# Performance work log

Measured on AMD Instinct MI355X. Metric: run time of the kernel, lower is better.

Reference implementation:

```python
import jax, jax.numpy as jnp
import numpy as np

N_NODES = 50000


def _sage_layer(h, src, dst, W_self, W_neigh, b):
    # DGL SAGEConv with 'mean' aggregator: fc_self(h) + fc_neigh(mean_{u in N(v)} h_u) + b
    msg = h[src]                                             # [E, d] gather
    agg = jax.ops.segment_sum(msg, dst, num_segments=N_NODES)  # [N, d]
    deg = jax.ops.segment_sum(jnp.ones((src.shape[0], 1), h.dtype), dst, num_segments=N_NODES)
    mean = agg / jnp.maximum(deg, 1.0)
    return h @ W_self + mean @ W_neigh + b


def _edge_mlp(h, src, dst, Wp1, bp1, Wp2, bp2):
    # MLPPredictor: score(u,v) = W2 relu(W1 [h_u ; h_v])
    z = jnp.concatenate([h[src], h[dst]], axis=-1)           # [Ep, 2*out]
    hdn = jax.nn.relu(z @ Wp1 + bp1)
    return (hdn @ Wp2 + bp2)[:, 0]                           # [Ep]


def setup_inputs() -> dict:
    key = jax.random.key(0)
    ks = jax.random.split(key, 16)
    N, E, EP = N_NODES, 160000, 100000
    d_in, d_h, d_out = 512, 256, 64

    def glorot(k, shape):
        fan = shape[0] + shape[1]
        return jax.random.normal(k, shape, jnp.float32) * jnp.sqrt(2.0 / fan)

    return {
        "x": jax.random.normal(ks[0], (N, d_in), jnp.float32),
        "edge_src": jax.random.randint(ks[1], (E,), 0, N, jnp.int32),
        "edge_dst": jax.random.randint(ks[2], (E,), 0, N, jnp.int32),
        "pos_src": jax.random.randint(ks[3], (EP,), 0, N, jnp.int32),
        "pos_dst": jax.random.randint(ks[4], (EP,), 0, N, jnp.int32),
        "neg_src": jax.random.randint(ks[5], (EP,), 0, N, jnp.int32),
        "neg_dst": jax.random.randint(ks[6], (EP,), 0, N, jnp.int32),
        "W_self1": glorot(ks[7], (d_in, d_h)),
        "W_neigh1": glorot(ks[8], (d_in, d_h)),
        "b1": jnp.zeros((d_h,), jnp.float32),
        "W_self2": glorot(ks[9], (d_h, d_out)),
        "W_neigh2": glorot(ks[10], (d_h, d_out)),
        "b2": jnp.zeros((d_out,), jnp.float32),
        "Wp1": glorot(ks[11], (2 * d_out, d_out)),
        "bp1": jnp.zeros((d_out,), jnp.float32),
        "Wp2": glorot(ks[12], (d_out, 1)),
        "bp2": jnp.zeros((1,), jnp.float32),
    }


def reference(x, edge_src, edge_dst, pos_src, pos_dst, neg_src, neg_dst,
              W_self1, W_neigh1, b1, W_self2, W_neigh2, b2, Wp1, bp1, Wp2, bp2):
    # 2-layer SAGE (512 -> 256 -> 64), relu between layers
    h = jax.nn.relu(_sage_layer(x, edge_src, edge_dst, W_self1, W_neigh1, b1))
    h = _sage_layer(h, edge_src, edge_dst, W_self2, W_neigh2, b2)
    pos_score = _edge_mlp(h, pos_src, pos_dst, Wp1, bp1, Wp2, bp2)
    neg_score = _edge_mlp(h, neg_src, neg_dst, Wp1, bp1, Wp2, bp2)
    return (pos_score, neg_score)
```

## Files before the change

### kernel.cpp

```cpp
#include <hip/hip_runtime.h>

#define NN 50000
#define NE 160000
#define NP 100000
#define DIN 512
#define DH  256
#define DO  64
#define NBLK_SCAN 196

#define PW1_BLKS 1024
#define PW2_BLKS 128
#define PWP_BLKS 32
#define ZDEG_BLKS 196
#define PREP_BLKS (PW1_BLKS + PW2_BLKS + PWP_BLKS + ZDEG_BLKS)

typedef short bf16x8 __attribute__((ext_vector_type(8)));
typedef float f32x4  __attribute__((ext_vector_type(4)));

__device__ __forceinline__ float bf2f(unsigned short u) {
    return __uint_as_float(((unsigned int)u) << 16);
}
__device__ __forceinline__ unsigned short f2bf(float f) {
    unsigned int x = __float_as_uint(f);
    return (unsigned short)((x + 0x7fffu + ((x >> 16) & 1u)) >> 16);
}

__device__ __forceinline__ void gload_lds16(const void* g, void* l) {
    __builtin_amdgcn_global_load_lds(
        (const __attribute__((address_space(1))) void*)g,
        (__attribute__((address_space(3))) void*)l, 16, 0, 0);
}

__global__ __launch_bounds__(256) void prep_all(
    const float* __restrict__ Wself1, const float* __restrict__ Wneigh1, unsigned short* __restrict__ Bt1,
    const float* __restrict__ Wself2, const float* __restrict__ Wneigh2, unsigned short* __restrict__ Bt2,
    const float* __restrict__ Wp1, unsigned short* __restrict__ Wp1b,
    int* __restrict__ deg_i)
{
    int blk = blockIdx.x;
    if (blk < PW1_BLKS) {
        int idx = blk * 256 + threadIdx.x;
        int n = idx >> 9, k = idx & 511;
        float v = (n < DH) ? Wself1[(size_t)k * DH + n] : Wneigh1[(size_t)k * DH + (n - DH)];
        Bt1[idx] = f2bf(v);
        return;
    }
    blk -= PW1_BLKS;
    if (blk < PW2_BLKS) {
        int idx = blk * 256 + threadIdx.x;
        int n = idx >> 8, k = idx & 255;
        float v = (n < DO) ? Wself2[(size_t)k * DO + n] : Wneigh2[(size_t)k * DO + (n - DO)];
        Bt2[idx] = f2bf(v);
        return;
    }
    blk -= PW2_BLKS;
    if (blk < PWP_BLKS) {
        int idx = blk * 256 + threadIdx.x;
        int n = idx >> 7, k = idx & 127;
        Wp1b[idx] = f2bf(Wp1[(size_t)k * 64 + n]);
        return;
    }
    blk -= PWP_BLKS;
    {
        int i = blk * 256 + threadIdx.x;
        if (i < 50048) deg_i[i] = 0;
    }
}

__global__ __launch_bounds__(256) void deg_count(const int* __restrict__ dst, int* __restrict__ deg) {
    int e = blockIdx.x * 256 + threadIdx.x;
    if (e < NE) atomicAdd(&deg[dst[e]], 1);
}

__global__ __launch_bounds__(256) void scan_part(const int* __restrict__ deg, int* __restrict__ excl,
                                                 int* __restrict__ bsums) {
    __shared__ int sh[256];
    int i = blockIdx.x * 256 + threadIdx.x;
    int v = (i < NN) ? deg[i] : 0;
    sh[threadIdx.x] = v;
    __syncthreads();
    #pragma unroll
    for (int off = 1; off < 256; off <<= 1) {
        int t = (threadIdx.x >= off) ? sh[threadIdx.x - off] : 0;
        __syncthreads();
        sh[threadIdx.x] += t;
        __syncthreads();
    }
    if (i < NN) excl[i] = sh[threadIdx.x] - v;
    if (threadIdx.x == 255) bsums[blockIdx.x] = sh[255];
}

__global__ __launch_bounds__(256) void scan_sums(int* __restrict__ bsums, int* __restrict__ boff) {
    __shared__ int sh[256];
    int v = (threadIdx.x < NBLK_SCAN) ? bsums[threadIdx.x] : 0;
    sh[threadIdx.x] = v;
    __syncthreads();
    #pragma unroll
    for (int off = 1; off < 256; off <<= 1) {
        int t = (threadIdx.x >= off) ? sh[threadIdx.x - off] : 0;
        __syncthreads();
        sh[threadIdx.x] += t;
        __syncthreads();
    }
    boff[threadIdx.x] = sh[threadIdx.x] - v;
}

__global__ __launch_bounds__(256) void scan_add(int* __restrict__ off, const int* __restrict__ boff,
                                                int* __restrict__ cursor) {
    int i = blockIdx.x * 256 + threadIdx.x;
    if (i < NN) {
        int o = off[i] + boff[blockIdx.x];
        off[i] = o;
        cursor[i] = o;
    }
    if (i == 0) off[NN] = NE;
}

__global__ __launch_bounds__(256) void fill_csr(const int* __restrict__ src, const int* __restrict__ dst,
                                                int* __restrict__ cursor, int* __restrict__ eidx) {
    int e = blockIdx.x * 256 + threadIdx.x;
    if (e < NE) {
        int p = atomicAdd(&cursor[dst[e]], 1);
        eidx[p] = src[e];
    }
}

__global__ __launch_bounds__(256) void gemm_xf32(
    const float* __restrict__ A, const unsigned short* __restrict__ Bt,
    unsigned short* __restrict__ Cout, int M, int N, int K)
{
    __shared__ unsigned short As[2][128 * 64];
    __shared__ unsigned short Bs[2][128 * 64];
    const int tid = threadIdx.x;
    const int w = tid >> 6, l = tid & 63;
    const int wr = (w >> 1) * 64, wc = (w & 1) * 64;

    const int nwg = gridDim.x, gx = N >> 7;
    const int q = nwg >> 3, r = nwg & 7;
    const int xcd = blockIdx.x & 7, pos = blockIdx.x >> 3;
    const int work = (xcd < r ? xcd * (q + 1) : r * (q + 1) + (xcd - r) * q) + pos;
    const int row0 = (work / gx) * 128, col0 = (work % gx) * 128;

    f32x4 acc[4][4];
    #pragma unroll
    for (int i = 0; i < 4; ++i)
        #pragma unroll
        for (int j = 0; j < 4; ++j)
            #pragma unroll
            for (int rr = 0; rr < 4; ++rr) acc[i][j][rr] = 0.0f;

    const int wave_lds_chunk = (tid & 192) * 8;

    float4 pa[4][2];

#define LOAD_PA(K0)                                                          \
    {                                                                        \
        _Pragma("unroll")                                                    \
        for (int u = 0; u < 4; ++u) {                                        \
            int c = u * 256 + tid;                                           \
            int row_ = c >> 3, j_ = c & 7;                                   \
            int grow = row0 + row_; if (grow >= M) grow = M - 1;             \
            const float* s = A + (size_t)grow * K + (K0) + j_ * 8;           \
            pa[u][0] = *(const float4*)s;                                    \
            pa[u][1] = *(const float4*)(s + 4);                              \
        }                                                                    \
    }

#define WRITE_A(BUF)                                                         \
    {                                                                        \
        _Pragma("unroll")                                                    \
        for (int u = 0; u < 4; ++u) {                                        \
            int c = u * 256 + tid;                                           \
            int row_ = c >> 3, j_ = c & 7;                                   \
            int js_ = j_ ^ (row_ & 7);                                       \
            union { bf16x8 v; unsigned int u32[4]; } pk;                     \
            asm("v_cvt_pk_bf16_f32 %0, %1, %2" : "=v"(pk.u32[0]) : "v"(pa[u][0].x), "v"(pa[u][0].y)); \
            asm("v_cvt_pk_bf16_f32 %0, %1, %2" : "=v"(pk.u32[1]) : "v"(pa[u][0].z), "v"(pa[u][0].w)); \
            asm("v_cvt_pk_bf16_f32 %0, %1, %2" : "=v"(pk.u32[2]) : "v"(pa[u][1].x), "v"(pa[u][1].y)); \
            asm("v_cvt_pk_bf16_f32 %0, %1, %2" : "=v"(pk.u32[3]) : "v"(pa[u][1].z), "v"(pa[u][1].w)); \
            *(bf16x8*)&As[BUF][row_ * 64 + js_ * 8] = pk.v;                  \
        }                                                                    \
    }

#define STAGE_B(BUF, K0)                                                     \
    {                                                                        \
        _Pragma("unroll")                                                    \
        for (int u = 0; u < 4; ++u) {                                        \
            int c = u * 256 + tid;                                           \
            int cn = c >> 3, j_ = c & 7;                                     \
            int js_ = j_ ^ (cn & 7);                                         \
            gload_lds16(Bt + (size_t)(col0 + cn) * K + (K0) + js_ * 8,       \
                        (void*)(Bs[BUF] + (u * 256) * 8 + wave_lds_chunk));  \
        }                                                                    \
    }

    LOAD_PA(0);
    STAGE_B(0, 0);
    WRITE_A(0);
    LOAD_PA(64);
    __syncthreads();

    int cur = 0;
    for (int k0 = 0; k0 < K; k0 += 64) {
        const int nxt = k0 + 64;
        if (nxt < K) {
            STAGE_B(cur ^ 1, nxt);
            WRITE_A(cur ^ 1);
            if (nxt + 64 < K) LOAD_PA(nxt + 64);
        }

        #pragma unroll
        for (int kk = 0; kk < 2; ++kk) {
            bf16x8 af[4], bfv[4];
            #pragma unroll
            for (int i = 0; i < 4; ++i) {
                int row = wr + i * 16 + (l & 15);
                int ch = (kk * 4 + (l >> 4)) ^ (row & 7);
                af[i] = *(const bf16x8*)&As[cur][row * 64 + ch * 8];
            }
            #pragma unroll
            for (int j = 0; j < 4; ++j) {
                int cc = wc + j * 16 + (l & 15);
                int ch = (kk * 4 + (l >> 4)) ^ (cc & 7);
                bfv[j] = *(const bf16x8*)&Bs[cur][cc * 64 + ch * 8];
            }
            #pragma unroll
            for (int i = 0; i < 4; ++i)
                #pragma unroll
                for (int j = 0; j < 4; ++j)
                    acc[i][j] = __builtin_amdgcn_mfma_f32_16x16x32_bf16(af[i], bfv[j], acc[i][j], 0, 0, 0);
        }
        __syncthreads();
        cur ^= 1;
    }
#undef LOAD_PA
#undef WRITE_A
#undef STAGE_B

    #pragma unroll
    for (int i = 0; i < 4; ++i) {
        #pragma unroll
        for (int j = 0; j < 4; ++j) {
            int r0 = row0 + wr + i * 16 + ((l >> 4) << 2);
            int c  = col0 + wc + j * 16 + (l & 15);
            #pragma unroll
            for (int rr = 0; rr < 4; ++rr) {
                if (r0 + rr < M)
                    Cout[(size_t)(r0 + rr) * N + c] = f2bf(acc[i][j][rr]);
            }
        }
    }
}

__global__ __launch_bounds__(256) void gemm_bf16(
    const unsigned short* __restrict__ A, const unsigned short* __restrict__ Bt,
    unsigned short* __restrict__ Cout, int M, int N, int K)
{
    __shared__ unsigned short As[128 * 64];
    __shared__ unsigned short Bs[128 * 64];
    const int tid = threadIdx.x;
    const int w = tid >> 6, l = tid & 63;
    const int wr = (w >> 1) * 64, wc = (w & 1) * 64;

    const int nwg = gridDim.x, gx = N >> 7;
    const int q = nwg >> 3, r = nwg & 7;
    const int xcd = blockIdx.x & 7, pos = blockIdx.x >> 3;
    const int work = (xcd < r ? xcd * (q + 1) : r * (q + 1) + (xcd - r) * q) + pos;
    const int row0 = (work / gx) * 128, col0 = (work % gx) * 128;

    f32x4 acc[4][4];
    #pragma unroll
    for (int i = 0; i < 4; ++i)
        #pragma unroll
        for (int j = 0; j < 4; ++j)
            #pragma unroll
            for (int rr = 0; rr < 4; ++rr) acc[i][j][rr] = 0.0f;

    const int wave_lds_chunk = (tid & 192) * 8;

    for (int k0 = 0; k0 < K; k0 += 64) {
        __syncthreads();
        #pragma unroll
        for (int u = 0; u < 4; ++u) {
            int c = u * 256 + tid;
            int row = c >> 3, j = c & 7;
            int js = j ^ (row & 7);
            int grow = row0 + row; if (grow >= M) grow = M - 1;
            gload_lds16(A + (size_t)grow * K + k0 + js * 8,
                        (void*)(As + (u * 256) * 8 + wave_lds_chunk));
        }
        #pragma unroll
        for (int u = 0; u < 4; ++u) {
            int c = u * 256 + tid;
            int cn = c >> 3, j = c & 7;
            int js = j ^ (cn & 7);
            gload_lds16(Bt + (size_t)(col0 + cn) * K + k0 + js * 8,
                        (void*)(Bs + (u * 256) * 8 + wave_lds_chunk));
        }
        __syncthreads();

        #pragma unroll
        for (int kk = 0; kk < 2; ++kk) {
            bf16x8 af[4], bfv[4];
            #pragma unroll
            for (int i = 0; i < 4; ++i) {
                int row = wr + i * 16 + (l & 15);
                int ch = (kk * 4 + (l >> 4)) ^ (row & 7);
                af[i] = *(const bf16x8*)&As[row * 64 + ch * 8];
            }
            #pragma unroll
            for (int j = 0; j < 4; ++j) {
                int cc = wc + j * 16 + (l & 15);
                int ch = (kk * 4 + (l >> 4)) ^ (cc & 7);
                bfv[j] = *(const bf16x8*)&Bs[cc * 64 + ch * 8];
            }
            #pragma unroll
            for (int i = 0; i < 4; ++i)
                #pragma unroll
                for (int j = 0; j < 4; ++j)
                    acc[i][j] = __builtin_amdgcn_mfma_f32_16x16x32_bf16(af[i], bfv[j], acc[i][j], 0, 0, 0);
        }
    }

    #pragma unroll
    for (int i = 0; i < 4; ++i) {
        #pragma unroll
        for (int j = 0; j < 4; ++j) {
            int r0 = row0 + wr + i * 16 + ((l >> 4) << 2);
            int c  = col0 + wc + j * 16 + (l & 15);
            #pragma unroll
            for (int rr = 0; rr < 4; ++rr) {
                if (r0 + rr < M)
                    Cout[(size_t)(r0 + rr) * N + c] = f2bf(acc[i][j][rr]);
            }
        }
    }
}

__global__ __launch_bounds__(256) void agg_combine256(
    const unsigned short* __restrict__ C1, const int* __restrict__ off, const int* __restrict__ eidx,
    const float* __restrict__ b, unsigned short* __restrict__ h1b)
{
    const int wave = threadIdx.x >> 6, lane = threadIdx.x & 63;
    const int n = blockIdx.x * 4 + wave;
    if (n >= NN) return;
    const int e0 = off[n], e1 = off[n + 1];
    float acc0 = 0.f, acc1 = 0.f, acc2 = 0.f, acc3 = 0.f;
    for (int e = e0; e < e1; ++e) {
        int s = eidx[e];
        ushort4 v = *(const ushort4*)&C1[(size_t)s * 512 + 256 + lane * 4];
        acc0 += bf2f(v.x); acc1 += bf2f(v.y); acc2 += bf2f(v.z); acc3 += bf2f(v.w);
    }
    const float rd = (e1 > e0) ? 1.0f / (float)(e1 - e0) : 1.0f;
    ushort4 sv = *(const ushort4*)&C1[(size_t)n * 512 + lane * 4];
    float4 bb = ((const float4*)b)[lane];
    ushort4 o;
    o.x = f2bf(fmaxf(bf2f(sv.x) + acc0 * rd + bb.x, 0.f));
    o.y = f2bf(fmaxf(bf2f(sv.y) + acc1 * rd + bb.y, 0.f));
    o.z = f2bf(fmaxf(bf2f(sv.z) + acc2 * rd + bb.z, 0.f));
    o.w = f2bf(fmaxf(bf2f(sv.w) + acc3 * rd + bb.w, 0.f));
    *(ushort4*)&h1b[(size_t)n * 256 + lane * 4] = o;
}

__global__ __launch_bounds__(256) void agg_combine64(
    const unsigned short* __restrict__ C2, const int* __restrict__ off, const int* __restrict__ eidx,
    const float* __restrict__ b, unsigned short* __restrict__ h2b)
{
    const int wave = threadIdx.x >> 6, lane = threadIdx.x & 63;
    const int n = blockIdx.x * 4 + wave;
    if (n >= NN) return;
    const int e0 = off[n], e1 = off[n + 1];
    float acc = 0.f;
    for (int e = e0; e < e1; ++e) {
        int s = eidx[e];
        acc += bf2f(C2[(size_t)s * 128 + 64 + lane]);
    }
    const float rd = (e1 > e0) ? 1.0f / (float)(e1 - e0) : 1.0f;
    h2b[(size_t)n * 64 + lane] = f2bf(bf2f(C2[(size_t)n * 128 + lane]) + acc * rd + b[lane]);
}

__global__ __launch_bounds__(256) void edge_mlp_mfma(
    const unsigned short* __restrict__ h2b,
    const int* __restrict__ psrc, const int* __restrict__ pdst,
    const int* __restrict__ nsrc, const int* __restrict__ ndst,
    const unsigned short* __restrict__ Wp1b, const float* __restrict__ bp1,
    const float* __restrict__ Wp2, const float* __restrict__ bp2,
    float* __restrict__ out)
{
    __shared__ unsigned short z[128 * 128];
    const int tid = threadIdx.x;
    const int w = tid >> 6, l = tid & 63;
    const int e0 = blockIdx.x * 128;

    bf16x8 bfr[4][4];
    #pragma unroll
    for (int kk = 0; kk < 4; ++kk)
        #pragma unroll
        for (int j = 0; j < 4; ++j) {
            int col = j * 16 + (l & 15);
            int ch  = kk * 4 + (l >> 4);
            bfr[kk][j] = *(const bf16x8*)(Wp1b + col * 128 + ch * 8);
        }

    #pragma unroll
    for (int p = 0; p < 8; ++p) {
        int rho = p * 32 + (tid >> 3);
        int c   = tid & 7;
        int r   = rho >> 1;
        int ep  = rho & 1;
        int e   = e0 + r; if (e >= 2 * NP) e = 2 * NP - 1;
        int node = (e < NP) ? (ep ? pdst[e] : psrc[e])
                            : (ep ? ndst[e - NP] : nsrc[e - NP]);
        bf16x8 v = *(const bf16x8*)(h2b + (size_t)node * 64 + c * 8);
        int j = ep * 8 + c;
        *(bf16x8*)&z[r * 128 + ((j ^ (r & 15)) * 8)] = v;
    }
    __syncthreads();

    f32x4 acc[2][4];
    #pragma unroll
    for (int i = 0; i < 2; ++i)
        #pragma unroll
        for (int j = 0; j < 4; ++j)
            #pragma unroll
            for (int rr = 0; rr < 4; ++rr) acc[i][j][rr] = 0.0f;

    #pragma unroll
    for (int kk = 0; kk < 4; ++kk) {
        bf16x8 af[2];
        #pragma unroll
        for (int i = 0; i < 2; ++i) {
            int row = w * 32 + i * 16 + (l & 15);
            int ch  = (kk * 4 + (l >> 4)) ^ (row & 15);
            af[i] = *(const bf16x8*)&z[row * 128 + ch * 8];
        }
        #pragma unroll
        for (int i = 0; i < 2; ++i)
            #pragma unroll
            for (int j = 0; j < 4; ++j)
                acc[i][j] = __builtin_amdgcn_mfma_f32_16x16x32_bf16(af[i], bfr[kk][j], acc[i][j], 0, 0, 0);
    }

    float bp1v[4], w2v[4];
    #pragma unroll
    for (int j = 0; j < 4; ++j) {
        bp1v[j] = bp1[j * 16 + (l & 15)];
        w2v[j]  = Wp2[j * 16 + (l & 15)];
    }
    const float b2v = bp2[0];
    #pragma unroll
    for (int i = 0; i < 2; ++i) {
        #pragma unroll
        for (int rr = 0; rr < 4; ++rr) {
            float p = 0.f;
            #pragma unroll
            for (int j = 0; j < 4; ++j) {
                float h = fmaxf(acc[i][j][rr] + bp1v[j], 0.f);
                p = fmaf(h, w2v[j], p);
            }
            #pragma unroll
            for (int off = 8; off > 0; off >>= 1)
                p += __shfl_xor(p, off, 64);
            int row = w * 32 + i * 16 + ((l >> 4) << 2) + rr;
            if ((l & 15) == 0 && e0 + row < 2 * NP)
                out[e0 + row] = p + b2v;
        }
    }
}

extern "C" void kernel_launch(void* const* d_in, const int* in_sizes, int n_in,
                              void* d_out, int out_size, void* d_ws, size_t ws_size,
                              hipStream_t stream) {
    (void)in_sizes; (void)n_in; (void)out_size; (void)ws_size;
    const float* x       = (const float*)d_in[0];
    const int*   esrc    = (const int*)d_in[1];
    const int*   edst    = (const int*)d_in[2];
    const int*   psrc    = (const int*)d_in[3];
    const int*   pdst    = (const int*)d_in[4];
    const int*   nsrc    = (const int*)d_in[5];
    const int*   ndst    = (const int*)d_in[6];
    const float* Wself1  = (const float*)d_in[7];
    const float* Wneigh1 = (const float*)d_in[8];
    const float* b1      = (const float*)d_in[9];
    const float* Wself2  = (const float*)d_in[10];
    const float* Wneigh2 = (const float*)d_in[11];
    const float* b2      = (const float*)d_in[12];
    const float* Wp1     = (const float*)d_in[13];
    const float* bp1     = (const float*)d_in[14];
    const float* Wp2     = (const float*)d_in[15];
    const float* bp2     = (const float*)d_in[16];
    float* out = (float*)d_out;

    char* w = (char*)d_ws;
    int* deg_i  = (int*)w; w += 50048 * 4;
    int* off    = (int*)w; w += 50052 * 4;
    int* cursor = (int*)w; w += 50048 * 4;
    int* bsums  = (int*)w; w += 256 * 4;
    int* boff   = (int*)w; w += 256 * 4;
    int* eidx   = (int*)w; w += 160000 * 4;
    unsigned short* Bt1  = (unsigned short*)w; w += (size_t)512 * 512 * 2;
    unsigned short* Bt2  = (unsigned short*)w; w += (size_t)128 * 256 * 2;
    unsigned short* Wp1b = (unsigned short*)w; w += (size_t)64 * 128 * 2;
    unsigned short* h1b  = (unsigned short*)w; w += (size_t)NN * DH * 2;
    unsigned short* h2b  = (unsigned short*)w; w += (size_t)NN * DO * 2;
    unsigned short* C1b  = (unsigned short*)w; w += (size_t)NN * 512 * 2;
    unsigned short* C2b  = C1b;

    prep_all<<<PREP_BLKS, 256, 0, stream>>>(Wself1, Wneigh1, Bt1,
                                            Wself2, Wneigh2, Bt2, Wp1, Wp1b, deg_i);

    deg_count<<<(NE + 255) / 256, 256, 0, stream>>>(edst, deg_i);
    scan_part<<<NBLK_SCAN, 256, 0, stream>>>(deg_i, off, bsums);
    scan_sums<<<1, 256, 0, stream>>>(bsums, boff);
    scan_add<<<NBLK_SCAN, 256, 0, stream>>>(off, boff, cursor);
    fill_csr<<<(NE + 255) / 256, 256, 0, stream>>>(esrc, edst, cursor, eidx);

    int nwg1 = (512 / 128) * ((NN + 127) / 128);
    gemm_xf32<<<nwg1, 256, 0, stream>>>(x, Bt1, C1b, NN, 512, DIN);
    agg_combine256<<<(NN + 3) / 4, 256, 0, stream>>>(C1b, off, eidx, b1, h1b);

    int nwg2 = (128 / 128) * ((NN + 127) / 128);
    gemm_bf16<<<nwg2, 256, 0, stream>>>(h1b, Bt2, C2b, NN, 128, DH);
    agg_combine64<<<(NN + 3) / 4, 256, 0, stream>>>(C2b, off, eidx, b2, h2b);

    edge_mlp_mfma<<<(2 * NP + 127) / 128, 256, 0, stream>>>(h2b, psrc, pdst, nsrc, ndst,
                                                            Wp1b, bp1, Wp2, bp2, out);
}
```

Before: 184.0 us.

## Switch layer-1 GEMM to single-buffered LDS with register prefetch of both operands

Replaces the double-buffered LDS scheme, where B was loaded straight into LDS asynchronously, with a single LDS buffer per operand. Both A and B tiles are now prefetched into registers one step ahead and written to LDS between two barriers each iteration. This halves LDS use, which may raise occupancy and drops the direct-to-LDS path, but it adds a second barrier per k-step and more register pressure for the B prefetch.

```diff
diff --git a/kernel.cpp b/kernel.cpp
--- a/kernel.cpp
+++ b/kernel.cpp
@@ -129,8 +129,8 @@
     const float* __restrict__ A, const unsigned short* __restrict__ Bt,
     unsigned short* __restrict__ Cout, int M, int N, int K)
 {
-    __shared__ unsigned short As[2][128 * 64];
-    __shared__ unsigned short Bs[2][128 * 64];
+    __shared__ unsigned short As[128 * 64];
+    __shared__ unsigned short Bs[128 * 64];
     const int tid = threadIdx.x;
     const int w = tid >> 6, l = tid & 63;
     const int wr = (w >> 1) * 64, wc = (w & 1) * 64;
@@ -149,9 +149,8 @@
             #pragma unroll
             for (int rr = 0; rr < 4; ++rr) acc[i][j][rr] = 0.0f;
 
-    const int wave_lds_chunk = (tid & 192) * 8;
-
     float4 pa[4][2];
+    bf16x8 pb[4];
 
 #define LOAD_PA(K0)                                                          \
     {                                                                        \
@@ -166,7 +165,17 @@
         }                                                                    \
     }
 
-#define WRITE_A(BUF)                                                         \
+#define LOAD_PB(K0)                                                          \
+    {                                                                        \
+        _Pragma("unroll")                                                    \
+        for (int u = 0; u < 4; ++u) {                                        \
+            int c = u * 256 + tid;                                           \
+            int cn_ = c >> 3, j_ = c & 7;                                    \
+            pb[u] = *(const bf16x8*)(Bt + (size_t)(col0 + cn_) * K + (K0) + j_ * 8); \
+        }                                                                    \
+    }
+
+#define WRITE_AB()                                                           \
     {                                                                        \
         _Pragma("unroll")                                                    \
         for (int u = 0; u < 4; ++u) {                                        \
@@ -178,35 +187,22 @@
             asm("v_cvt_pk_bf16_f32 %0, %1, %2" : "=v"(pk.u32[1]) : "v"(pa[u][0].z), "v"(pa[u][0].w)); \
             asm("v_cvt_pk_bf16_f32 %0, %1, %2" : "=v"(pk.u32[2]) : "v"(pa[u][1].x), "v"(pa[u][1].y)); \
             asm("v_cvt_pk_bf16_f32 %0, %1, %2" : "=v"(pk.u32[3]) : "v"(pa[u][1].z), "v"(pa[u][1].w)); \
-            *(bf16x8*)&As[BUF][row_ * 64 + js_ * 8] = pk.v;                  \
+            *(bf16x8*)&As[row_ * 64 + js_ * 8] = pk.v;                       \
+            *(bf16x8*)&Bs[row_ * 64 + js_ * 8] = pb[u];                      \
         }                                                                    \
     }
 
-#define STAGE_B(BUF, K0)                                                     \
-    {                                                                        \
-        _Pragma("unroll")                                                    \
-        for (int u = 0; u < 4; ++u) {                                        \
-            int c = u * 256 + tid;                                           \
-            int cn = c >> 3, j_ = c & 7;                                     \
-            int js_ = j_ ^ (cn & 7);                                         \
-            gload_lds16(Bt + (size_t)(col0 + cn) * K + (K0) + js_ * 8,       \
-                        (void*)(Bs[BUF] + (u * 256) * 8 + wave_lds_chunk));  \
-        }                                                                    \
-    }
-
     LOAD_PA(0);
-    STAGE_B(0, 0);
-    WRITE_A(0);
-    LOAD_PA(64);
-    __syncthreads();
-
-    int cur = 0;
+    LOAD_PB(0);
+
     for (int k0 = 0; k0 < K; k0 += 64) {
-        const int nxt = k0 + 64;
-        if (nxt < K) {
-            STAGE_B(cur ^ 1, nxt);
-            WRITE_A(cur ^ 1);
-            if (nxt + 64 < K) LOAD_PA(nxt + 64);
+        __syncthreads();
+        WRITE_AB();
+        __syncthreads();
+
+        if (k0 + 64 < K) {
+            LOAD_PA(k0 + 64);
+            LOAD_PB(k0 + 64);
         }
 
         #pragma unroll
@@ -216,13 +212,13 @@
             for (int i = 0; i < 4; ++i) {
                 int row = wr + i * 16 + (l & 15);
                 int ch = (kk * 4 + (l >> 4)) ^ (row & 7);
-                af[i] = *(const bf16x8*)&As[cur][row * 64 + ch * 8];
+                af[i] = *(const bf16x8*)&As[row * 64 + ch * 8];
             }
             #pragma unroll
             for (int j = 0; j < 4; ++j) {
                 int cc = wc + j * 16 + (l & 15);
                 int ch = (kk * 4 + (l >> 4)) ^ (cc & 7);
-                bfv[j] = *(const bf16x8*)&Bs[cur][cc * 64 + ch * 8];
+                bfv[j] = *(const bf16x8*)&Bs[cc * 64 + ch * 8];
             }
             #pragma unroll
             for (int i = 0; i < 4; ++i)
@@ -230,12 +226,10 @@
                 for (int j = 0; j < 4; ++j)
                     acc[i][j] = __builtin_amdgcn_mfma_f32_16x16x32_bf16(af[i], bfv[j], acc[i][j], 0, 0, 0);
         }
-        __syncthreads();
-        cur ^= 1;
     }
 #undef LOAD_PA
-#undef WRITE_A
-#undef STAGE_B
+#undef LOAD_PB
+#undef WRITE_AB
 
     #pragma unroll
     for (int i = 0; i < 4; ++i) {
```

After: 182.3 us. About the same (-0.9%).
